# Optimization experiments

Hardware: AMD Instinct MI355X
Metric: run time of the kernel (lower is better)

## Reference

```python
import jax, jax.numpy as jnp
import numpy as np

D, FH, FW = 41, 16, 44          # depth bins (arange(4,45,1)), feat H/W = 256/16, 704/16
NX, NY, NZ = 128, 128, 1        # BEV grid from grid_conf
C_CTX = 64                      # LSS context channels
EPS = 1e-5


def _frustum():
    ds = jnp.arange(4.0, 45.0, 1.0)                 # (D,)
    xs = jnp.linspace(0.0, 703.0, FW)
    ys = jnp.linspace(0.0, 255.0, FH)
    return jnp.stack([
        jnp.broadcast_to(xs[None, None, :], (D, FH, FW)),
        jnp.broadcast_to(ys[None, :, None], (D, FH, FW)),
        jnp.broadcast_to(ds[:, None, None], (D, FH, FW)),
    ], -1)                                           # (D,FH,FW,3)


def _bn(x, g, b, m, v):
    # inference-mode BatchNorm2d, x: (B,C,H,W)
    scale = g / jnp.sqrt(v + EPS)
    return x * scale[None, :, None, None] + (b - m * scale)[None, :, None, None]


def setup_inputs() -> dict:
    key = jax.random.key(0)
    ks = jax.random.split(key, 24)
    B, N = 4, 6
    imgs = jax.random.normal(ks[0], (B, N, 3, 256, 704), jnp.float32)
    eye = jnp.eye(3, dtype=jnp.float32)
    # well-conditioned camera matrices (code takes torch.inverse of these)
    rots = eye + 0.05 * jax.random.normal(ks[1], (B, N, 3, 3), jnp.float32)
    trans = 2.0 * jax.random.normal(ks[2], (B, N, 3), jnp.float32)
    K = jnp.array([[500., 0., 352.], [0., 500., 128.], [0., 0., 1.]], jnp.float32)
    kmask = jnp.array([[1., 0., 1.], [0., 1., 1.], [0., 0., 0.]], jnp.float32)
    intrins = K + 5.0 * jax.random.normal(ks[3], (B, N, 3, 3), jnp.float32) * kmask
    post_rots = eye + 0.01 * jax.random.normal(ks[4], (B, N, 3, 3), jnp.float32)
    post_trans = jax.random.normal(ks[5], (B, N, 3), jnp.float32)
    # backbone: Conv2d(3,256,16,16) + BN(256)
    conv_w = 0.02 * jax.random.normal(ks[6], (256, 3, 16, 16), jnp.float32)
    conv_b = 0.01 * jax.random.normal(ks[7], (256,), jnp.float32)
    bn1_g = 1.0 + 0.1 * jax.random.normal(ks[8], (256,), jnp.float32)
    bn1_b = 0.1 * jax.random.normal(ks[9], (256,), jnp.float32)
    bn1_m = 0.1 * jax.random.normal(ks[10], (256,), jnp.float32)
    bn1_v = jax.random.uniform(ks[11], (256,), jnp.float32, 0.5, 1.5)
    # depth_net: Conv2d(256, D+64=105, 1)
    depth_w = 0.05 * jax.random.normal(ks[12], (D + C_CTX, 256), jnp.float32)
    depth_b = 0.01 * jax.random.normal(ks[13], (D + C_CTX,), jnp.float32)
    # BEV encoder: Conv2d(128,64,3,pad=1) + BN(64)
    enc_w = 0.05 * jax.random.normal(ks[14], (64, 128, 3, 3), jnp.float32)
    enc_b = 0.01 * jax.random.normal(ks[15], (64,), jnp.float32)
    bn2_g = 1.0 + 0.1 * jax.random.normal(ks[16], (64,), jnp.float32)
    bn2_b = 0.1 * jax.random.normal(ks[17], (64,), jnp.float32)
    bn2_m = 0.1 * jax.random.normal(ks[18], (64,), jnp.float32)
    bn2_v = jax.random.uniform(ks[19], (64,), jnp.float32, 0.5, 1.5)
    # head: Conv2d(64, 7, 1)
    head_w = 0.05 * jax.random.normal(ks[20], (7, 64), jnp.float32)
    head_b = 0.01 * jax.random.normal(ks[21], (7,), jnp.float32)
    return dict(curr_imgs=imgs, rots=rots, trans=trans, intrins=intrins,
                post_rots=post_rots, post_trans=post_trans,
                conv_w=conv_w, conv_b=conv_b, bn1_g=bn1_g, bn1_b=bn1_b,
                bn1_m=bn1_m, bn1_v=bn1_v, depth_w=depth_w, depth_b=depth_b,
                enc_w=enc_w, enc_b=enc_b, bn2_g=bn2_g, bn2_b=bn2_b,
                bn2_m=bn2_m, bn2_v=bn2_v, head_w=head_w, head_b=head_b)


def _forward(curr_imgs, rots, trans, intrins, post_rots, post_trans,
             conv_w, conv_b, bn1_g, bn1_b, bn1_m, bn1_v,
             depth_w, depth_b, enc_w, enc_b, bn2_g, bn2_b, bn2_m, bn2_v,
             head_w, head_b):
    B, N = curr_imgs.shape[:2]
    dn = ('NCHW', 'OIHW', 'NCHW')
    # backbone (patchify conv + BN + ReLU)
    x = curr_imgs.reshape(B * N, 3, 256, 704)
    x = jax.lax.conv_general_dilated(x, conv_w, (16, 16), 'VALID', dimension_numbers=dn)
    x = jax.nn.relu(_bn(x + conv_b[None, :, None, None], bn1_g, bn1_b, bn1_m, bn1_v))  # (BN,256,16,44)
    # depth net (1x1 conv) -> depth softmax + context
    y = jnp.einsum('oc,bchw->bohw', depth_w, x) + depth_b[None, :, None, None]
    depth = jax.nn.softmax(y[:, :D], axis=1)                 # (BN,D,H,W)
    ctx = y[:, D:]                                           # (BN,C,H,W)
    # LSS outer product: (BN,C,D,H,W) -> (B,N,D,H,W,C)
    outer = ctx[:, :, None] * depth[:, None]
    outer = outer.reshape(B, N, C_CTX, D, FH, FW).transpose(0, 1, 3, 4, 5, 2)
    # geometry: pixel frustum -> ego coords
    fr = _frustum()                                          # (D,FH,FW,3)
    pts = fr[None, None] - post_trans[:, :, None, None, None, :]
    pts = jnp.einsum('bnij,bndhwj->bndhwi', jnp.linalg.inv(post_rots), pts)
    pts = jnp.concatenate([pts[..., :2] * pts[..., 2:3], pts[..., 2:3]], -1)
    comb = rots @ jnp.linalg.inv(intrins)
    pts = jnp.einsum('bnij,bndhwj->bndhwi', comb, pts) + trans[:, :, None, None, None, :]
    # voxel pooling (segment-sum == sort+cumsum trick of the original)
    dx = jnp.array([0.8, 0.8, 20.0], jnp.float32)
    low = jnp.array([-51.2, -51.2, -10.0], jnp.float32)      # bx - dx/2
    coords = ((pts.reshape(-1, 3) - low) / dx).astype(jnp.int32)  # trunc-to-zero like .long()
    rank = coords[:, 0] + coords[:, 1] * NX + coords[:, 2] * NX * NY
    tot = NX * NY * NZ
    kept = (rank >= 0) & (rank < tot)                        # combined-rank check only (as in source)
    feats = outer.reshape(-1, C_CTX) * kept[:, None].astype(outer.dtype)
    bev_flat = jax.ops.segment_sum(feats, jnp.where(kept, rank, 0), num_segments=tot)
    bev = bev_flat.reshape(NZ, NY, NX, C_CTX).transpose(0, 3, 1, 2)  # (1,64,128,128); batch mixed as in source
    # temporal fusion (prev_bev=None branch): cat(bev, bev)
    feat = jnp.concatenate([bev, bev], 1)                    # (1,128,128,128)
    feat = jax.lax.conv_general_dilated(feat, enc_w, (1, 1), 'SAME', dimension_numbers=dn)
    feat = jax.nn.relu(_bn(feat + enc_b[None, :, None, None], bn2_g, bn2_b, bn2_m, bn2_v))
    out = jnp.einsum('oc,bchw->bohw', head_w, feat) + head_b[None, :, None, None]
    return out, bev


def reference(curr_imgs, rots, trans, intrins, post_rots, post_trans,
              conv_w, conv_b, bn1_g, bn1_b, bn1_m, bn1_v,
              depth_w, depth_b, enc_w, enc_b, bn2_g, bn2_b, bn2_m, bn2_v,
              head_w, head_b):
    return _forward(curr_imgs, rots, trans, intrins, post_rots, post_trans,
                    conv_w, conv_b, bn1_g, bn1_b, bn1_m, bn1_v,
                    depth_w, depth_b, enc_w, enc_b, bn2_g, bn2_b, bn2_m, bn2_v,
                    head_w, head_b)
```

## Files before the change

kernel.cpp:

```cpp
#include <hip/hip_runtime.h>
#include <hip/hip_bf16.h>
#include <hip/hip_fp16.h>

#define NPTS 692736
#define NPATCH 16896

typedef _Float16 h16;
typedef __attribute__((ext_vector_type(4))) _Float16 half4v;
typedef __attribute__((ext_vector_type(8))) _Float16 half8v;
typedef __attribute__((ext_vector_type(4))) float f32x4;

__device__ float  v11_xbuf[NPATCH*256];
__device__ float  v11_ctx[NPATCH*64];
__device__ float  v11_depth[NPATCH*41];
__device__ int    v11_ranks[NPTS];
__device__ float  v11_bev[16384*64];
__device__ double v11_geom[24*24];

__device__ h16    v18_whi[196608];
__device__ h16    v18_wlo[196608];

__device__ h16    v15_dwhi[112*256];
__device__ h16    v15_dwlo[112*256];

__device__ h16    v16_w2hi[64*576];
__device__ h16    v16_w2lo[64*576];

__device__ int    v12_cnt[16384];
__device__ int    v12_off[16384];
__device__ int    v12_pos[NPTS];
__device__ int2   v12_sorted[NPTS];
__device__ int    v12_total;

__device__ __forceinline__ void inv3_v11(const double* m, double* o){
  double a=m[0],b=m[1],c=m[2],d=m[3],e=m[4],f=m[5],g=m[6],h=m[7],i=m[8];
  double A = e*i - f*h, B = -(d*i - f*g), C = d*h - e*g;
  double det = a*A + b*B + c*C;
  double id = 1.0/det;
  o[0]=A*id;            o[1]=-(b*i - c*h)*id; o[2]=(b*f - c*e)*id;
  o[3]=B*id;            o[4]=(a*i - c*g)*id;  o[5]=-(a*f - c*d)*id;
  o[6]=C*id;            o[7]=-(a*h - b*g)*id; o[8]=(a*e - b*d)*id;
}

__global__ void zero_v13(){
  int gid = blockIdx.x*256 + threadIdx.x;
  v11_bev[gid] = 0.f;
  if (gid < 16384) v12_cnt[gid] = 0;
}

__global__ void geom_v11(const float* rots, const float* trans, const float* intrins,
                         const float* post_rots, const float* post_trans){
  int t = threadIdx.x;
  if (t >= 24) return;
  double pr[9], it[9], r[9];
  for (int i=0;i<9;i++){
    pr[i] = (double)post_rots[t*9+i];
    it[i] = (double)intrins[t*9+i];
    r[i]  = (double)rots[t*9+i];
  }
  double ipr[9], iit[9];
  inv3_v11(pr, ipr); inv3_v11(it, iit);
  double* g = v11_geom + t*24;
  for (int i=0;i<3;i++) for(int j=0;j<3;j++){
    double s=0; for(int k=0;k<3;k++) s += r[i*3+k]*iit[k*3+j];
    g[9+i*3+j]=s;
  }
  for (int i=0;i<9;i++) g[i]   = ipr[i];
  for (int i=0;i<3;i++) g[18+i]= (double)post_trans[t*3+i];
  for (int i=0;i<3;i++) g[21+i]= (double)trans[t*3+i];
}

__global__ void wt_v18(const float* cw){
  int gid = blockIdx.x*256 + threadIdx.x;
  int e  = gid & 7;
  int t  = gid >> 3;
  int o  = t & 127;
  int t2 = t >> 7;
  int kc = t2 & 7;
  int t3 = t2 >> 3;
  int kt = t3 % 12;
  int ob = t3 / 12;
  int k  = kt*64 + kc*8 + e;
  int oc = ob*128 + o;
  float x = cw[oc*768 + k];
  h16 hi = (h16)x;
  h16 lo = (h16)(x - (float)hi);
  v18_whi[gid] = hi;
  v18_wlo[gid] = lo;
}

__global__ void wtd_v15(const float* dw){
  int gid = blockIdx.x*256 + threadIdx.x;
  int o = gid >> 8, c = gid & 255;
  float x = (o < 105) ? dw[o*256 + c] : 0.f;
  h16 hi = (h16)x;
  h16 lo = (h16)(x - (float)hi);
  v15_dwhi[gid] = hi;
  v15_dwlo[gid] = lo;
}

__global__ void w2_v16(const float* enc_w){
  int gid = blockIdx.x*256 + threadIdx.x;
  if (gid >= 36864) return;
  int o = gid / 576; int k = gid % 576;
  int tap = k >> 6, ic = k & 63;
  float x = enc_w[o*1152 + ic*9 + tap] + enc_w[o*1152 + (ic+64)*9 + tap];
  h16 hi = (h16)x;
  h16 lo = (h16)(x - (float)hi);
  v16_w2hi[gid] = hi;
  v16_w2lo[gid] = lo;
}

__global__ __launch_bounds__(256) void conv1_v18(const float* img,
    const float* cb, const float* g1, const float* b1, const float* m1, const float* v1){
  __shared__ __align__(16) h16 Ah[8][64][8];
  __shared__ __align__(16) h16 Al[8][64][8];
  __shared__ __align__(16) h16 Bh[8192];
  __shared__ __align__(16) h16 Bl[8192];
  int tid  = threadIdx.x;
  int lane = tid & 63, wv = tid >> 6;
  int wr = wv >> 1, wc = wv & 1;
  int pbase = blockIdx.x * 64;

  int pp0 = tid >> 3, kc0 = tid & 7;
  const float* ab[2];
  #pragma unroll
  for (int i=0;i<2;i++){
    int p = pbase + pp0 + 32*i;
    int im = p/704, pix = p%704;
    int ph = pix/44, pw = pix%44;
    ab[i] = img + (size_t)im*540672 + (size_t)ph*16*704 + pw*16;
  }

  f32x4 acc[2][4];
  #pragma unroll
  for (int mf=0;mf<2;mf++)
    #pragma unroll
    for (int nf=0;nf<4;nf++) acc[mf][nf] = (f32x4){0.f,0.f,0.f,0.f};

  int fr = lane & 15, fg = lane >> 4;

  for (int ktI=0; ktI<12; ktI++){
    int kt = ktI*64;
    __syncthreads();
    {
      int k0 = kt + kc0*8;
      int c = k0>>8, rem = k0&255, ky = rem>>4, kx = rem&15;
      size_t goff = (size_t)c*180224 + ky*704 + kx;
      #pragma unroll
      for (int i=0;i<2;i++){
        int pp = pp0 + 32*i;
        const float* src = ab[i] + goff;
        float4 v0 = *(const float4*)src;
        float4 v1 = *(const float4*)(src+4);
        float vv[8] = {v0.x,v0.y,v0.z,v0.w,v1.x,v1.y,v1.z,v1.w};
        half8v hv, lv;
        #pragma unroll
        for (int e=0;e<8;e++){ h16 h=(h16)vv[e]; hv[e]=h; lv[e]=(h16)(vv[e]-(float)h); }
        int srow = pp ^ kc0;
        *(half8v*)&Ah[kc0][srow][0] = hv;
        *(half8v*)&Al[kc0][srow][0] = lv;
      }
    }
    {
      const h16* ph = v18_whi + (size_t)(blockIdx.y*12 + ktI)*8192;
      const h16* pl = v18_wlo + (size_t)(blockIdx.y*12 + ktI)*8192;
      #pragma unroll
      for (int i=0;i<4;i++){
        int l = tid + i*256;
        *(half8v*)&Bh[l*8] = *(const half8v*)(ph + l*8);
        *(half8v*)&Bl[l*8] = *(const half8v*)(pl + l*8);
      }
    }
    __syncthreads();
    #pragma unroll
    for (int ks=0;ks<2;ks++){
      int kc = ks*4 + fg;
      half8v ah[2], al[2], bh[4], bl[4];
      #pragma unroll
      for (int mf=0;mf<2;mf++){
        int row = (wr*32 + mf*16 + fr) ^ kc;
        ah[mf] = *(const half8v*)&Ah[kc][row][0];
        al[mf] = *(const half8v*)&Al[kc][row][0];
      }
      #pragma unroll
      for (int nf=0;nf<4;nf++){
        int col = wc*64 + nf*16 + fr;
        bh[nf] = *(const half8v*)&Bh[(kc*128 + col)*8];
        bl[nf] = *(const half8v*)&Bl[(kc*128 + col)*8];
      }
      #pragma unroll
      for (int mf=0;mf<2;mf++)
        #pragma unroll
        for (int nf=0;nf<4;nf++){
          acc[mf][nf] = __builtin_amdgcn_mfma_f32_16x16x32_f16(ah[mf], bh[nf], acc[mf][nf], 0,0,0);
          acc[mf][nf] = __builtin_amdgcn_mfma_f32_16x16x32_f16(ah[mf], bl[nf], acc[mf][nf], 0,0,0);
          acc[mf][nf] = __builtin_amdgcn_mfma_f32_16x16x32_f16(al[mf], bh[nf], acc[mf][nf], 0,0,0);
        }
    }
  }
  int obase = blockIdx.y * 128;
  #pragma unroll
  for (int nf=0;nf<4;nf++){
    int ch = obase + wc*64 + nf*16 + fr;
    float sc = g1[ch] / sqrtf(v1[ch] + 1e-5f);
    float sh = b1[ch] - m1[ch]*sc;
    float bi = cb[ch];
    #pragma unroll
    for (int mf=0;mf<2;mf++){
      #pragma unroll
      for (int j=0;j<4;j++){
        int pq = pbase + wr*32 + mf*16 + fg*4 + j;
        float t = (acc[mf][nf][j] + bi)*sc + sh;
        v11_xbuf[(size_t)pq*256 + ch] = t > 0.f ? t : 0.f;
      }
    }
  }
}

__global__ __launch_bounds__(256) void depth_v16(const float* db){
  __shared__ __align__(16) h16 Ah[4][64][8];
  __shared__ __align__(16) h16 Al[4][64][8];
  __shared__ __align__(16) h16 Bh[4][112][8];
  __shared__ __align__(16) h16 Bl[4][112][8];
  __shared__ float sy[64*113];
  int tid = threadIdx.x;
  int lane = tid & 63, wv = tid >> 6;
  int pbase = blockIdx.x*64;
  int fr = lane & 15, fg = lane >> 4;

  int app = tid & 63;
  int kcA = tid >> 6;
  const float* xsrc = &v11_xbuf[(size_t)(pbase+app)*256 + kcA*8];

  f32x4 acc[7];
  #pragma unroll
  for (int nf=0;nf<7;nf++) acc[nf] = (f32x4){0.f,0.f,0.f,0.f};

  for (int kt=0; kt<256; kt+=32){
    __syncthreads();
    {
      float4 v0 = *(const float4*)(xsrc + kt);
      float4 v1 = *(const float4*)(xsrc + kt + 4);
      float vv[8] = {v0.x,v0.y,v0.z,v0.w,v1.x,v1.y,v1.z,v1.w};
      half8v hv, lv;
      #pragma unroll
      for (int e=0;e<8;e++){ h16 h=(h16)vv[e]; hv[e]=h; lv[e]=(h16)(vv[e]-(float)h); }
      *(half8v*)&Ah[kcA][app][0] = hv;
      *(half8v*)&Al[kcA][app][0] = lv;
    }
    for (int l = tid; l < 448; l += 256){
      int kc = l/112, o = l%112;
      *(half8v*)&Bh[kc][o][0] = *(const half8v*)&v15_dwhi[o*256 + kt + kc*8];
      *(half8v*)&Bl[kc][o][0] = *(const half8v*)&v15_dwlo[o*256 + kt + kc*8];
    }
    __syncthreads();
    int row = wv*16 + fr;
    half8v ah = *(const half8v*)&Ah[fg][row][0];
    half8v al = *(const half8v*)&Al[fg][row][0];
    #pragma unroll
    for (int nf=0;nf<7;nf++){
      int col = nf*16 + fr;
      half8v bh = *(const half8v*)&Bh[fg][col][0];
      half8v bl = *(const half8v*)&Bl[fg][col][0];
      acc[nf] = __builtin_amdgcn_mfma_f32_16x16x32_f16(ah, bh, acc[nf], 0,0,0);
      acc[nf] = __builtin_amdgcn_mfma_f32_16x16x32_f16(ah, bl, acc[nf], 0,0,0);
      acc[nf] = __builtin_amdgcn_mfma_f32_16x16x32_f16(al, bh, acc[nf], 0,0,0);
    }
  }
  #pragma unroll
  for (int nf=0;nf<7;nf++){
    int o = nf*16 + fr;
    if (o < 105){
      float bias = db[o];
      #pragma unroll
      for (int j=0;j<4;j++){
        int pp = wv*16 + fg*4 + j;
        sy[pp*113 + o] = acc[nf][j] + bias;
      }
    }
  }
  __syncthreads();
  if (tid < 64){
    float* y = &sy[tid*113];
    float m = y[0];
    for (int i=1;i<41;i++) m = fmaxf(m, y[i]);
    float s = 0.f;
    for (int i=0;i<41;i++){ float e = expf(y[i]-m); y[i] = e; s += e; }
    float inv = 1.f/s;
    for (int i=0;i<41;i++) y[i] *= inv;
  }
  __syncthreads();
  for (int l = tid; l < 64*41; l += 256){
    int pp = l/41, dd = l%41;
    v11_depth[(size_t)(pbase+pp)*41 + dd] = sy[pp*113+dd];
  }
  for (int l = tid; l < 64*64; l += 256){
    int pp = l>>6, c = l&63;
    v11_ctx[(size_t)(pbase+pp)*64 + c] = sy[pp*113 + 41 + c];
  }
}

__global__ __launch_bounds__(256) void rank_v13(){
  __shared__ int lh[16384];
  int tid = threadIdx.x;
  for (int i = tid; i < 16384; i += 256) lh[i] = 0;
  __syncthreads();
  int base = blockIdx.x*1024;
  int rk[4], lp[4];
  #pragma unroll
  for (int k=0;k<4;k++){
    int idx = base + k*256 + tid;
    rk[k] = -1; lp[k] = 0;
    if (idx < NPTS){
      int im = idx / 28864;
      int r  = idx % 28864;
      int d  = r / 704; int pix = r % 704;
      int h = pix / 44, w = pix % 44;
      const double* g = v11_geom + im*24;
      double fx = (double)w * (703.0/43.0);
      double fy = (double)h * 17.0;
      double fz = 4.0 + (double)d;
      double px = fx - g[18], py = fy - g[19], pz = fz - g[20];
      double q0 = g[0]*px + g[1]*py + g[2]*pz;
      double q1 = g[3]*px + g[4]*py + g[5]*pz;
      double q2 = g[6]*px + g[7]*py + g[8]*pz;
      q0 *= q2; q1 *= q2;
      double o0 = g[9]*q0  + g[10]*q1 + g[11]*q2 + g[21];
      double o1 = g[12]*q0 + g[13]*q1 + g[14]*q2 + g[22];
      double o2 = g[15]*q0 + g[16]*q1 + g[17]*q2 + g[23];
      int cx = (int)((o0 + 51.2)/0.8);
      int cy = (int)((o1 + 51.2)/0.8);
      int cz = (int)((o2 + 10.0)/20.0);
      int rank = cx + cy*128 + cz*16384;
      if (rank >= 0 && rank < 16384){
        rk[k] = rank;
        lp[k] = atomicAdd(&lh[rank], 1);
      }
    }
  }
  __syncthreads();
  for (int i = tid; i < 16384; i += 256){
    int h = lh[i];
    if (h) lh[i] = atomicAdd(&v12_cnt[i], h);
  }
  __syncthreads();
  #pragma unroll
  for (int k=0;k<4;k++){
    int idx = base + k*256 + tid;
    if (idx < NPTS){
      v11_ranks[idx] = rk[k];
      if (rk[k] >= 0) v12_pos[idx] = lh[rk[k]] + lp[k];
    }
  }
}

__global__ __launch_bounds__(256) void scan_v13(){
  __shared__ int part[256];
  int t = threadIdx.x;
  int base = t*64;
  int s = 0;
  for (int i=0;i<64;i++) s += v12_cnt[base+i];
  part[t] = s;
  __syncthreads();
  if (t == 0){
    int run = 0;
    for (int i=0;i<256;i++){ int v = part[i]; part[i] = run; run += v; }
    v12_total = run;
  }
  __syncthreads();
  int run = part[t];
  for (int i=0;i<64;i++){
    v12_off[base+i] = run;
    run += v12_cnt[base+i];
  }
}

__global__ __launch_bounds__(256) void fill_v13(){
  int idx = blockIdx.x*256 + threadIdx.x;
  if (idx >= NPTS) return;
  int rank = v11_ranks[idx];
  if (rank < 0) return;
  int im = idx / 28864;
  int r  = idx % 28864;
  int d  = r / 704; int pix = r % 704;
  int p  = im*704 + pix;
  int pos = v12_off[rank] + v12_pos[idx];
  v12_sorted[pos] = make_int2((p<<6) | d, rank);
}

__global__ __launch_bounds__(256) void gather_v13(){
  int total = v12_total;
  int w = threadIdx.x >> 6;
  int chunk = blockIdx.x*256 + w*64;
  if (chunk >= total) return;
  int lane = threadIdx.x & 63;
  int n = total - chunk; if (n > 64) n = 64;
  int pv = 0, rv = -1;
  float dv = 0.f;
  if (lane < n){
    int2 sr = v12_sorted[chunk + lane];
    pv = sr.x; rv = sr.y;
    dv = v11_depth[(pv>>6)*41 + (pv & 63)];
  }
  float acc = 0.f;
  int cur = __shfl(rv, 0);
  for (int i = 0; i < n; i++){
    int rk = __shfl(rv, i);
    int pp = __shfl(pv, i) >> 6;
    float dd = __shfl(dv, i);
    if (rk != cur){
      atomicAdd(&v11_bev[(size_t)cur*64 + lane], acc);
      acc = 0.f; cur = rk;
    }
    acc += v11_ctx[(pp<<6) | lane] * dd;
  }
  atomicAdd(&v11_bev[(size_t)cur*64 + lane], acc);
}

__global__ void bevout_v11(float* out1){
  int gid = blockIdx.x*256 + threadIdx.x;
  int c  = gid >> 14;
  int yx = gid & 16383;
  out1[gid] = v11_bev[(size_t)yx*64 + c];
}

__global__ __launch_bounds__(256) void conv2_v17(
    const float* eb, const float* g2, const float* b2_, const float* m2, const float* v2,
    const float* hw, const float* hb, float* out0){
  __shared__ __align__(16) h16 Ah[4][64][8];
  __shared__ __align__(16) h16 Al[4][64][8];
  __shared__ __align__(16) h16 Bh[4][64][8];
  __shared__ __align__(16) h16 Bl[4][64][8];
  __shared__ float sfeat[64*68];
  __shared__ float hred[4*64*7];
  int tid = threadIdx.x;
  int lane = tid & 63, wv = tid >> 6;
  int bx = blockIdx.x & 15, by = blockIdx.x >> 4;
  int fr = lane & 15, fg = lane >> 4;

  int app = tid & 63;
  int kcT = tid >> 6;
  int apy = app >> 3, apx = app & 7;

  f32x4 acc[4];
  #pragma unroll
  for (int nf=0;nf<4;nf++) acc[nf] = (f32x4){0.f,0.f,0.f,0.f};

  for (int kt=0; kt<576; kt+=32){
    int tap = kt >> 6, ic0 = kt & 32;
    int dy = tap/3 - 1, dx = tap%3 - 1;
    __syncthreads();
    {
      int gy = by*8 + apy + dy, gx = bx*8 + apx + dx;
      float4 v0 = {0.f,0.f,0.f,0.f}, v1 = {0.f,0.f,0.f,0.f};
      if (gy>=0 && gy<128 && gx>=0 && gx<128){
        const float* src = &v11_bev[(size_t)(gy*128+gx)*64 + ic0 + kcT*8];
        v0 = *(const float4*)src;
        v1 = *(const float4*)(src+4);
      }
      float vv[8] = {v0.x,v0.y,v0.z,v0.w,v1.x,v1.y,v1.z,v1.w};
      half8v hv, lv;
      #pragma unroll
      for (int e=0;e<8;e++){ h16 h=(h16)vv[e]; hv[e]=h; lv[e]=(h16)(vv[e]-(float)h); }
      *(half8v*)&Ah[kcT][app][0] = hv;
      *(half8v*)&Al[kcT][app][0] = lv;
    }
    {
      *(half8v*)&Bh[kcT][app][0] = *(const half8v*)&v16_w2hi[app*576 + kt + kcT*8];
      *(half8v*)&Bl[kcT][app][0] = *(const half8v*)&v16_w2lo[app*576 + kt + kcT*8];
    }
    __syncthreads();
    int row = wv*16 + fr;
    half8v ah = *(const half8v*)&Ah[fg][row][0];
    half8v al = *(const half8v*)&Al[fg][row][0];
    #pragma unroll
    for (int nf=0;nf<4;nf++){
      int col = nf*16 + fr;
      half8v bh = *(const half8v*)&Bh[fg][col][0];
      half8v bl = *(const half8v*)&Bl[fg][col][0];
      acc[nf] = __builtin_amdgcn_mfma_f32_16x16x32_f16(ah, bh, acc[nf], 0,0,0);
      acc[nf] = __builtin_amdgcn_mfma_f32_16x16x32_f16(ah, bl, acc[nf], 0,0,0);
      acc[nf] = __builtin_amdgcn_mfma_f32_16x16x32_f16(al, bh, acc[nf], 0,0,0);
    }
  }
  #pragma unroll
  for (int nf=0;nf<4;nf++){
    int ch = nf*16 + fr;
    float sc = g2[ch]/sqrtf(v2[ch]+1e-5f);
    float sh = b2_[ch] - m2[ch]*sc;
    float bi = eb[ch];
    #pragma unroll
    for (int j=0;j<4;j++){
      int pp = wv*16 + fg*4 + j;
      float t = (acc[nf][j] + bi)*sc + sh;
      sfeat[pp*68 + ch] = t > 0.f ? t : 0.f;
    }
  }
  __syncthreads();
  int og = tid >> 6, pix = tid & 63;
  float part[7];
  #pragma unroll
  for (int o=0;o<7;o++) part[o]=0.f;
  #pragma unroll
  for (int j=0;j<16;j++){
    int oc = og*16 + j;
    float v = sfeat[pix*68 + oc];
    #pragma unroll
    for (int o=0;o<7;o++) part[o] += hw[o*64+oc]*v;
  }
  #pragma unroll
  for (int o=0;o<7;o++) hred[(og*64+pix)*7+o] = part[o];
  __syncthreads();
  if (og == 0){
    int gy = by*8 + (pix>>3), gx = bx*8 + (pix&7);
    #pragma unroll
    for (int o=0;o<7;o++){
      float s = hred[pix*7+o] + hred[(64+pix)*7+o] + hred[(128+pix)*7+o]
              + hred[(192+pix)*7+o] + hb[o];
      out0[o*16384 + gy*128 + gx] = s;
    }
  }
}

extern "C" void kernel_launch(void* const* d_in, const int* in_sizes, int n_in,
                              void* d_out, int out_size, void* d_ws, size_t ws_size,
                              hipStream_t stream){
  const float* imgs       = (const float*)d_in[0];
  const float* rots       = (const float*)d_in[1];
  const float* trans      = (const float*)d_in[2];
  const float* intrins    = (const float*)d_in[3];
  const float* post_rots  = (const float*)d_in[4];
  const float* post_trans = (const float*)d_in[5];
  const float* conv_w     = (const float*)d_in[6];
  const float* conv_b     = (const float*)d_in[7];
  const float* bn1_g      = (const float*)d_in[8];
  const float* bn1_b      = (const float*)d_in[9];
  const float* bn1_m      = (const float*)d_in[10];
  const float* bn1_v      = (const float*)d_in[11];
  const float* depth_w    = (const float*)d_in[12];
  const float* depth_b    = (const float*)d_in[13];
  const float* enc_w      = (const float*)d_in[14];
  const float* enc_b      = (const float*)d_in[15];
  const float* bn2_g      = (const float*)d_in[16];
  const float* bn2_b      = (const float*)d_in[17];
  const float* bn2_m      = (const float*)d_in[18];
  const float* bn2_v      = (const float*)d_in[19];
  const float* head_w     = (const float*)d_in[20];
  const float* head_b     = (const float*)d_in[21];

  float* out0 = (float*)d_out;
  float* out1 = out0 + 114688;

  zero_v13<<<4096, 256, 0, stream>>>();
  geom_v11<<<1, 32, 0, stream>>>(rots, trans, intrins, post_rots, post_trans);
  wt_v18<<<768, 256, 0, stream>>>(conv_w);
  wtd_v15<<<112, 256, 0, stream>>>(depth_w);
  w2_v16<<<144, 256, 0, stream>>>(enc_w);
  conv1_v18<<<dim3(264, 2), 256, 0, stream>>>(imgs, conv_b, bn1_g, bn1_b, bn1_m, bn1_v);
  depth_v16<<<264, 256, 0, stream>>>(depth_b);
  rank_v13<<<(NPTS+1023)/1024, 256, 0, stream>>>();
  scan_v13<<<1, 256, 0, stream>>>();
  fill_v13<<<NPTS/256, 256, 0, stream>>>();
  gather_v13<<<NPTS/256, 256, 0, stream>>>();
  bevout_v11<<<4096, 256, 0, stream>>>(out1);
  conv2_v17<<<256, 256, 0, stream>>>(enc_b, bn2_g, bn2_b, bn2_m, bn2_v,
                                     head_w, head_b, out0);
}
```

Baseline: 264.4 us.

## Prefetch conv1 tiles into registers and drop LDS staging in depth/conv2

In conv1, the next K-tile's image and weight data are loaded into registers before the MFMA loop of the current tile, so global-load latency overlaps with compute (register prefetch double-buffering). The depth and conv2 GEMMs no longer stage through shared memory: each lane loads its MFMA A/B fragments directly from global memory, which removes the syncthreads and LDS traffic. The cost is higher register pressure in conv1, and in depth/conv2 the weight fragments are re-read from global/L2 by every wave instead of being shared.

```diff
diff --git a/kernel.cpp b/kernel.cpp
--- a/kernel.cpp
+++ b/kernel.cpp
@@ -111,7 +111,7 @@
   v16_w2lo[gid] = lo;
 }
 
-__global__ __launch_bounds__(256) void conv1_v18(const float* img,
+__global__ __launch_bounds__(256) void conv1_v19(const float* img,
     const float* cb, const float* g1, const float* b1, const float* m1, const float* v1){
   __shared__ __align__(16) h16 Ah[8][64][8];
   __shared__ __align__(16) h16 Al[8][64][8];
@@ -131,6 +131,32 @@
     int ph = pix/44, pw = pix%44;
     ab[i] = img + (size_t)im*540672 + (size_t)ph*16*704 + pw*16;
   }
+  const h16* wph = v18_whi + (size_t)blockIdx.y*12*8192;
+  const h16* wpl = v18_wlo + (size_t)blockIdx.y*12*8192;
+
+  float4 pa0[2], pa1[2];
+  half8v pbh[4], pbl[4];
+
+  auto LOAD_A = [&](int ktI){
+    int k0 = ktI*64 + kc0*8;
+    int c = k0>>8, rem = k0&255, ky = rem>>4, kx = rem&15;
+    size_t goff = (size_t)c*180224 + ky*704 + kx;
+    #pragma unroll
+    for (int i=0;i<2;i++){
+      pa0[i] = *(const float4*)(ab[i] + goff);
+      pa1[i] = *(const float4*)(ab[i] + goff + 4);
+    }
+  };
+  auto LOAD_B = [&](int ktI){
+    const h16* ph = wph + (size_t)ktI*8192;
+    const h16* pl = wpl + (size_t)ktI*8192;
+    #pragma unroll
+    for (int i=0;i<4;i++){
+      int l = tid + i*256;
+      pbh[i] = *(const half8v*)(ph + l*8);
+      pbl[i] = *(const half8v*)(pl + l*8);
+    }
+  };
 
   f32x4 acc[2][4];
   #pragma unroll
@@ -140,39 +166,29 @@
 
   int fr = lane & 15, fg = lane >> 4;
 
+  LOAD_A(0); LOAD_B(0);
+
   for (int ktI=0; ktI<12; ktI++){
-    int kt = ktI*64;
     __syncthreads();
-    {
-      int k0 = kt + kc0*8;
-      int c = k0>>8, rem = k0&255, ky = rem>>4, kx = rem&15;
-      size_t goff = (size_t)c*180224 + ky*704 + kx;
+    #pragma unroll
+    for (int i=0;i<2;i++){
+      float vv[8] = {pa0[i].x,pa0[i].y,pa0[i].z,pa0[i].w,
+                     pa1[i].x,pa1[i].y,pa1[i].z,pa1[i].w};
+      half8v hv, lv;
       #pragma unroll
-      for (int i=0;i<2;i++){
-        int pp = pp0 + 32*i;
-        const float* src = ab[i] + goff;
-        float4 v0 = *(const float4*)src;
-        float4 v1 = *(const float4*)(src+4);
-        float vv[8] = {v0.x,v0.y,v0.z,v0.w,v1.x,v1.y,v1.z,v1.w};
-        half8v hv, lv;
-        #pragma unroll
-        for (int e=0;e<8;e++){ h16 h=(h16)vv[e]; hv[e]=h; lv[e]=(h16)(vv[e]-(float)h); }
-        int srow = pp ^ kc0;
-        *(half8v*)&Ah[kc0][srow][0] = hv;
-        *(half8v*)&Al[kc0][srow][0] = lv;
-      }
-    }
-    {
-      const h16* ph = v18_whi + (size_t)(blockIdx.y*12 + ktI)*8192;
-      const h16* pl = v18_wlo + (size_t)(blockIdx.y*12 + ktI)*8192;
-      #pragma unroll
-      for (int i=0;i<4;i++){
-        int l = tid + i*256;
-        *(half8v*)&Bh[l*8] = *(const half8v*)(ph + l*8);
-        *(half8v*)&Bl[l*8] = *(const half8v*)(pl + l*8);
-      }
+      for (int e=0;e<8;e++){ h16 h=(h16)vv[e]; hv[e]=h; lv[e]=(h16)(vv[e]-(float)h); }
+      int srow = (pp0 + 32*i) ^ kc0;
+      *(half8v*)&Ah[kc0][srow][0] = hv;
+      *(half8v*)&Al[kc0][srow][0] = lv;
+    }
+    #pragma unroll
+    for (int i=0;i<4;i++){
+      int l = tid + i*256;
+      *(half8v*)&Bh[l*8] = pbh[i];
+      *(half8v*)&Bl[l*8] = pbl[i];
     }
     __syncthreads();
+    if (ktI < 11){ LOAD_A(ktI+1); LOAD_B(ktI+1); }
     #pragma unroll
     for (int ks=0;ks<2;ks++){
       int kc = ks*4 + fg;
@@ -218,51 +234,31 @@
   }
 }
 
-__global__ __launch_bounds__(256) void depth_v16(const float* db){
-  __shared__ __align__(16) h16 Ah[4][64][8];
-  __shared__ __align__(16) h16 Al[4][64][8];
-  __shared__ __align__(16) h16 Bh[4][112][8];
-  __shared__ __align__(16) h16 Bl[4][112][8];
+__global__ __launch_bounds__(256) void depth_v17(const float* db){
   __shared__ float sy[64*113];
   int tid = threadIdx.x;
   int lane = tid & 63, wv = tid >> 6;
   int pbase = blockIdx.x*64;
   int fr = lane & 15, fg = lane >> 4;
 
-  int app = tid & 63;
-  int kcA = tid >> 6;
-  const float* xsrc = &v11_xbuf[(size_t)(pbase+app)*256 + kcA*8];
+  const float* arow = &v11_xbuf[(size_t)(pbase + wv*16 + fr)*256 + fg*8];
 
   f32x4 acc[7];
   #pragma unroll
   for (int nf=0;nf<7;nf++) acc[nf] = (f32x4){0.f,0.f,0.f,0.f};
 
   for (int kt=0; kt<256; kt+=32){
-    __syncthreads();
-    {
-      float4 v0 = *(const float4*)(xsrc + kt);
-      float4 v1 = *(const float4*)(xsrc + kt + 4);
-      float vv[8] = {v0.x,v0.y,v0.z,v0.w,v1.x,v1.y,v1.z,v1.w};
-      half8v hv, lv;
-      #pragma unroll
-      for (int e=0;e<8;e++){ h16 h=(h16)vv[e]; hv[e]=h; lv[e]=(h16)(vv[e]-(float)h); }
-      *(half8v*)&Ah[kcA][app][0] = hv;
-      *(half8v*)&Al[kcA][app][0] = lv;
-    }
-    for (int l = tid; l < 448; l += 256){
-      int kc = l/112, o = l%112;
-      *(half8v*)&Bh[kc][o][0] = *(const half8v*)&v15_dwhi[o*256 + kt + kc*8];
-      *(half8v*)&Bl[kc][o][0] = *(const half8v*)&v15_dwlo[o*256 + kt + kc*8];
-    }
-    __syncthreads();
-    int row = wv*16 + fr;
-    half8v ah = *(const half8v*)&Ah[fg][row][0];
-    half8v al = *(const half8v*)&Al[fg][row][0];
+    float4 v0 = *(const float4*)(arow + kt);
+    float4 v1 = *(const float4*)(arow + kt + 4);
+    float vv[8] = {v0.x,v0.y,v0.z,v0.w,v1.x,v1.y,v1.z,v1.w};
+    half8v ah, al;
+    #pragma unroll
+    for (int e=0;e<8;e++){ h16 h=(h16)vv[e]; ah[e]=h; al[e]=(h16)(vv[e]-(float)h); }
     #pragma unroll
     for (int nf=0;nf<7;nf++){
-      int col = nf*16 + fr;
-      half8v bh = *(const half8v*)&Bh[fg][col][0];
-      half8v bl = *(const half8v*)&Bl[fg][col][0];
+      int off = (nf*16 + fr)*256 + kt + fg*8;
+      half8v bh = *(const half8v*)&v15_dwhi[off];
+      half8v bl = *(const half8v*)&v15_dwlo[off];
       acc[nf] = __builtin_amdgcn_mfma_f32_16x16x32_f16(ah, bh, acc[nf], 0,0,0);
       acc[nf] = __builtin_amdgcn_mfma_f32_16x16x32_f16(ah, bl, acc[nf], 0,0,0);
       acc[nf] = __builtin_amdgcn_mfma_f32_16x16x32_f16(al, bh, acc[nf], 0,0,0);
@@ -425,13 +421,9 @@
   out1[gid] = v11_bev[(size_t)yx*64 + c];
 }
 
-__global__ __launch_bounds__(256) void conv2_v17(
+__global__ __launch_bounds__(256) void conv2_v18(
     const float* eb, const float* g2, const float* b2_, const float* m2, const float* v2,
     const float* hw, const float* hb, float* out0){
-  __shared__ __align__(16) h16 Ah[4][64][8];
-  __shared__ __align__(16) h16 Al[4][64][8];
-  __shared__ __align__(16) h16 Bh[4][64][8];
-  __shared__ __align__(16) h16 Bl[4][64][8];
   __shared__ float sfeat[64*68];
   __shared__ float hred[4*64*7];
   int tid = threadIdx.x;
@@ -439,9 +431,8 @@
   int bx = blockIdx.x & 15, by = blockIdx.x >> 4;
   int fr = lane & 15, fg = lane >> 4;
 
-  int app = tid & 63;
-  int kcT = tid >> 6;
-  int apy = app >> 3, apx = app & 7;
+  int row = wv*16 + fr;
+  int py = row >> 3, px = row & 7;
 
   f32x4 acc[4];
   #pragma unroll
@@ -450,35 +441,22 @@
   for (int kt=0; kt<576; kt+=32){
     int tap = kt >> 6, ic0 = kt & 32;
     int dy = tap/3 - 1, dx = tap%3 - 1;
-    __syncthreads();
-    {
-      int gy = by*8 + apy + dy, gx = bx*8 + apx + dx;
-      float4 v0 = {0.f,0.f,0.f,0.f}, v1 = {0.f,0.f,0.f,0.f};
-      if (gy>=0 && gy<128 && gx>=0 && gx<128){
-        const float* src = &v11_bev[(size_t)(gy*128+gx)*64 + ic0 + kcT*8];
-        v0 = *(const float4*)src;
-        v1 = *(const float4*)(src+4);
-      }
-      float vv[8] = {v0.x,v0.y,v0.z,v0.w,v1.x,v1.y,v1.z,v1.w};
-      half8v hv, lv;
-      #pragma unroll
-      for (int e=0;e<8;e++){ h16 h=(h16)vv[e]; hv[e]=h; lv[e]=(h16)(vv[e]-(float)h); }
-      *(half8v*)&Ah[kcT][app][0] = hv;
-      *(half8v*)&Al[kcT][app][0] = lv;
-    }
-    {
-      *(half8v*)&Bh[kcT][app][0] = *(const half8v*)&v16_w2hi[app*576 + kt + kcT*8];
-      *(half8v*)&Bl[kcT][app][0] = *(const half8v*)&v16_w2lo[app*576 + kt + kcT*8];
-    }
-    __syncthreads();
-    int row = wv*16 + fr;
-    half8v ah = *(const half8v*)&Ah[fg][row][0];
-    half8v al = *(const half8v*)&Al[fg][row][0];
+    int gy = by*8 + py + dy, gx = bx*8 + px + dx;
+    float4 v0 = {0.f,0.f,0.f,0.f}, v1 = {0.f,0.f,0.f,0.f};
+    if (gy>=0 && gy<128 && gx>=0 && gx<128){
+      const float* src = &v11_bev[(size_t)(gy*128+gx)*64 + ic0 + fg*8];
+      v0 = *(const float4*)src;
+      v1 = *(const float4*)(src+4);
+    }
+    float vv[8] = {v0.x,v0.y,v0.z,v0.w,v1.x,v1.y,v1.z,v1.w};
+    half8v ah, al;
+    #pragma unroll
+    for (int e=0;e<8;e++){ h16 h=(h16)vv[e]; ah[e]=h; al[e]=(h16)(vv[e]-(float)h); }
     #pragma unroll
     for (int nf=0;nf<4;nf++){
-      int col = nf*16 + fr;
-      half8v bh = *(const half8v*)&Bh[fg][col][0];
-      half8v bl = *(const half8v*)&Bl[fg][col][0];
+      int off = (nf*16 + fr)*576 + kt + fg*8;
+      half8v bh = *(const half8v*)&v16_w2hi[off];
+      half8v bl = *(const half8v*)&v16_w2lo[off];
       acc[nf] = __builtin_amdgcn_mfma_f32_16x16x32_f16(ah, bh, acc[nf], 0,0,0);
       acc[nf] = __builtin_amdgcn_mfma_f32_16x16x32_f16(ah, bl, acc[nf], 0,0,0);
       acc[nf] = __builtin_amdgcn_mfma_f32_16x16x32_f16(al, bh, acc[nf], 0,0,0);
@@ -557,13 +535,13 @@
   wt_v18<<<768, 256, 0, stream>>>(conv_w);
   wtd_v15<<<112, 256, 0, stream>>>(depth_w);
   w2_v16<<<144, 256, 0, stream>>>(enc_w);
-  conv1_v18<<<dim3(264, 2), 256, 0, stream>>>(imgs, conv_b, bn1_g, bn1_b, bn1_m, bn1_v);
-  depth_v16<<<264, 256, 0, stream>>>(depth_b);
+  conv1_v19<<<dim3(264, 2), 256, 0, stream>>>(imgs, conv_b, bn1_g, bn1_b, bn1_m, bn1_v);
+  depth_v17<<<264, 256, 0, stream>>>(depth_b);
   rank_v13<<<(NPTS+1023)/1024, 256, 0, stream>>>();
   scan_v13<<<1, 256, 0, stream>>>();
   fill_v13<<<NPTS/256, 256, 0, stream>>>();
   gather_v13<<<NPTS/256, 256, 0, stream>>>();
   bevout_v11<<<4096, 256, 0, stream>>>(out1);
-  conv2_v17<<<256, 256, 0, stream>>>(enc_b, bn2_g, bn2_b, bn2_m, bn2_v,
+  conv2_v18<<<256, 256, 0, stream>>>(enc_b, bn2_g, bn2_b, bn2_m, bn2_v,
                                      head_w, head_b, out0);
 }
```

Result: slower. 285.8 us (+8.1%).
